# Performance work log

Measured on AMD Instinct MI355X. Metric: run time of the kernel, lower is better.

The kernel has to match this reference:

```python
import jax, jax.numpy as jnp
import numpy as np

EMBED_DIM = 1024
NUM_HEADS = 16
HEAD_DIM = EMBED_DIM // NUM_HEADS
ROPE_BASE = 10000.0


def _rope_cos_sin(seq_len, head_dim, dtype):
    # Standard RoPE (ESM-style rotate_half): freqs outer(t, inv_freq), emb = cat(freqs, freqs)
    inv_freq = 1.0 / (ROPE_BASE ** (jnp.arange(0, head_dim, 2, dtype=jnp.float32) / head_dim))
    t = jnp.arange(seq_len, dtype=jnp.float32)
    freqs = jnp.einsum('s,d->sd', t, inv_freq)          # [s, d/2]
    emb = jnp.concatenate([freqs, freqs], axis=-1)      # [s, d]
    return jnp.cos(emb).astype(dtype), jnp.sin(emb).astype(dtype)


def _rotate_half(x):
    x1, x2 = jnp.split(x, 2, axis=-1)
    return jnp.concatenate([-x2, x1], axis=-1)


def _apply_rope(x, cos, sin):
    # x: [b, h, s, d]; cos/sin: [s, d] broadcast over b, h
    return x * cos + _rotate_half(x) * sin


def setup_inputs() -> dict:
    key = jax.random.key(0)
    ks = jax.random.split(key, 5)
    b, s, e = 4, 2048, EMBED_DIM
    scale = 1.0 / np.sqrt(e)
    x = jax.random.normal(ks[0], (b, s, e), dtype=jnp.float32)
    Wqkv = jax.random.normal(ks[1], (e, 3 * e), dtype=jnp.float32) * scale
    bqkv = jnp.zeros((3 * e,), dtype=jnp.float32)
    Wo = jax.random.normal(ks[2], (e, e), dtype=jnp.float32) * scale
    bo = jnp.zeros((e,), dtype=jnp.float32)
    return {"x": x, "Wqkv": Wqkv, "bqkv": bqkv, "Wo": Wo, "bo": bo}


def reference(x, Wqkv, bqkv, Wo, bo):
    b, s, e = x.shape
    h, d = NUM_HEADS, HEAD_DIM
    qkv = jnp.einsum('bse,ef->bsf', x, Wqkv) + bqkv          # [b, s, 3e]
    q, k, v = jnp.split(qkv, 3, axis=-1)
    # b s (h d) -> b h s d
    q = q.reshape(b, s, h, d).transpose(0, 2, 1, 3)
    k = k.reshape(b, s, h, d).transpose(0, 2, 1, 3)
    v = v.reshape(b, s, h, d).transpose(0, 2, 1, 3)
    cos, sin = _rope_cos_sin(s, d, x.dtype)
    q = _apply_rope(q, cos, sin)
    k = _apply_rope(k, cos, sin)
    # scaled dot product attention (no mask, no dropout, non-causal)
    scores = jnp.einsum('bhqd,bhkd->bhqk', q, k) / jnp.asarray(np.sqrt(d), x.dtype)
    attn = jax.nn.softmax(scores, axis=-1)
    out = jnp.einsum('bhqk,bhkd->bhqd', attn, v)             # [b, h, s, d]
    out = out.transpose(0, 2, 1, 3).reshape(b, s, e)         # b h s d -> b s (h d)
    return jnp.einsum('bse,ef->bsf', out, Wo) + bo
```

## Files before the change

kernel.cpp:

```cpp
#include <hip/hip_runtime.h>
#include <stdint.h>
#include <stddef.h>

typedef __bf16 bf16;
typedef __attribute__((ext_vector_type(8))) __bf16 bf16x8;
typedef __attribute__((ext_vector_type(4))) __bf16 bf16x4;
typedef __attribute__((ext_vector_type(4))) float f32x4;
typedef __attribute__((ext_vector_type(4))) float float4v;

#define BATCH 4
#define SEQ   2048
#define EMB   1024
#define NH    16
#define HD    64
#define F3    3072

#define MFMA16(a, b, c) __builtin_amdgcn_mfma_f32_16x16x32_bf16((a), (b), (c), 0, 0, 0)

__device__ __forceinline__ void gload_lds16(const bf16* g, bf16* l) {
  __builtin_amdgcn_global_load_lds(
      (const __attribute__((address_space(1))) uint32_t*)g,
      (__attribute__((address_space(3))) uint32_t*)l, 16, 0, 0);
}

__global__ __launch_bounds__(256) void rope_table(float* __restrict__ cosT,
                                                  float* __restrict__ sinT) {
  int idx = blockIdx.x * 256 + threadIdx.x;
  int pos = idx >> 5, d1 = idx & 31;
  float inv = powf(10000.0f, -(float)(2 * d1) / 64.0f);
  float th = (float)pos * inv;
  cosT[idx] = cosf(th);
  sinT[idx] = sinf(th);
}

__global__ __launch_bounds__(256) void convert_bf16(const float* __restrict__ src,
                                                    bf16* __restrict__ dst, int n4) {
  int i = blockIdx.x * 256 + threadIdx.x;
  if (i >= n4) return;
  float4v v = ((const float4v*)src)[i];
  bf16x4 o;
#pragma unroll
  for (int k = 0; k < 4; ++k) o[k] = (bf16)v[k];
  ((bf16x4*)dst)[i] = o;
}

__global__ __launch_bounds__(256) void transpose_f32_bf16(const float* __restrict__ in,
                                                          bf16* __restrict__ out,
                                                          int R, int C) {
  __shared__ bf16 tile[32][33];
  const int tx = threadIdx.x & 31;
  const int ty = threadIdx.x >> 5;
  const int c0 = blockIdx.x * 32, r0 = blockIdx.y * 32;
#pragma unroll
  for (int kk = 0; kk < 4; ++kk) {
    int r = ty + kk * 8;
    tile[r][tx] = (bf16)in[(size_t)(r0 + r) * C + c0 + tx];
  }
  __syncthreads();
#pragma unroll
  for (int kk = 0; kk < 4; ++kk) {
    int r = ty + kk * 8;
    out[(size_t)(c0 + r) * R + r0 + tx] = tile[tx][r];
  }
}

__global__ __launch_bounds__(256) void qkv_rope_kernel(
    const bf16* __restrict__ x, const bf16* __restrict__ wT,
    const float* __restrict__ bias, bf16* __restrict__ qo, bf16* __restrict__ ko,
    bf16* __restrict__ vo, const float* __restrict__ cosT,
    const float* __restrict__ sinT) {
  __shared__ __align__(16) bf16 As[128 * 32];
  __shared__ __align__(16) bf16 Bs[128 * 32];
  const int tid = threadIdx.x;
  const int w = tid >> 6, lane = tid & 63;
  const int lhi = lane >> 4, llo = lane & 15;
  const int wr = w >> 1, wc = w & 1;
  const int row_a0 = blockIdx.y * 128;
  const int row_b0 = blockIdx.x * 128;

  f32x4 acc[4][4];
#pragma unroll
  for (int i = 0; i < 4; ++i)
#pragma unroll
    for (int j = 0; j < 4; ++j) acc[i][j] = (f32x4){0.f, 0.f, 0.f, 0.f};

  for (int k0 = 0; k0 < EMB; k0 += 32) {
#pragma unroll
    for (int c = 0; c < 2; ++c) {
      int chunk = w * 2 + c;
      int gl = chunk * 64 + lane;
      int row = gl >> 2, kk = (gl & 3) << 3;
      gload_lds16(x + (size_t)(row_a0 + row) * EMB + k0 + kk, &As[chunk * 512]);
      gload_lds16(wT + (size_t)(row_b0 + row) * EMB + k0 + kk, &Bs[chunk * 512]);
    }
    __syncthreads();
    bf16x8 a[4], b[4];
#pragma unroll
    for (int i = 0; i < 4; ++i)
      a[i] = *(const bf16x8*)&As[(wr * 64 + i * 16 + llo) * 32 + lhi * 8];
#pragma unroll
    for (int j = 0; j < 4; ++j)
      b[j] = *(const bf16x8*)&Bs[(wc * 64 + j * 16 + llo) * 32 + lhi * 8];
#pragma unroll
    for (int i = 0; i < 4; ++i)
#pragma unroll
      for (int j = 0; j < 4; ++j) acc[i][j] = MFMA16(a[i], b[j], acc[i][j]);
    __syncthreads();
  }

  const int f0 = row_b0 + wc * 64;
  const int part = f0 >> 10;
  const int hh = (f0 & 1023) >> 6;
  const int m_base = row_a0 + wr * 64;

  float bvals[4];
#pragma unroll
  for (int j = 0; j < 4; ++j) bvals[j] = bias[f0 + j * 16 + llo];

  if (part == 2) {
#pragma unroll
    for (int i = 0; i < 4; ++i) {
      int m0 = m_base + i * 16 + lhi * 4;
      int bb = m0 >> 11, pos0 = m0 & 2047;
#pragma unroll
      for (int j = 0; j < 4; ++j) {
        int dd = j * 16 + llo;
        bf16x4 pk;
#pragma unroll
        for (int r = 0; r < 4; ++r) pk[r] = (bf16)(acc[i][j][r] + bvals[j]);
        *(bf16x4*)(vo + ((size_t)(bb * NH + hh) * HD + dd) * SEQ + pos0) = pk;
      }
    }
  } else {
    bf16* dst = (part == 0) ? qo : ko;
    const float qs = (part == 0) ? 0.125f : 1.0f;
#pragma unroll
    for (int i = 0; i < 4; ++i) {
#pragma unroll
      for (int r = 0; r < 4; ++r) {
        int m = m_base + i * 16 + lhi * 4 + r;
        int bb = m >> 11, pos = m & 2047;
        size_t base = ((size_t)(bb * NH + hh) * SEQ + pos) * HD;
#pragma unroll
        for (int j = 0; j < 2; ++j) {
          int d1 = j * 16 + llo;
          float x1 = acc[i][j][r] + bvals[j];
          float x2 = acc[i][j + 2][r] + bvals[j + 2];
          float cth = cosT[pos * 32 + d1];
          float sth = sinT[pos * 32 + d1];
          dst[base + d1] = (bf16)((x1 * cth - x2 * sth) * qs);
          dst[base + d1 + 32] = (bf16)((x2 * cth + x1 * sth) * qs);
        }
      }
    }
  }
}

__global__ __launch_bounds__(512) void attn_kernel(const bf16* __restrict__ q,
                                                   const bf16* __restrict__ k,
                                                   const bf16* __restrict__ vT,
                                                   bf16* __restrict__ o) {
  __shared__ __align__(16) bf16 smem[32768];
  bf16* Qs = smem;

  const int tid = threadIdx.x, w = tid >> 6, lane = tid & 63;
  const int lhi = lane >> 4, llo = lane & 15;
  const int l7 = llo & 7;
  const int bidx = blockIdx.x;
  const int vblk = (bidx & 7) * 64 + (bidx >> 3);
  const int qt = vblk & 7, bh = vblk >> 3;
  const bf16* qbase = q + (size_t)bh * SEQ * HD + qt * 256 * HD;
  const bf16* kbase = k + (size_t)bh * SEQ * HD;
  const bf16* vbase = vT + (size_t)bh * HD * SEQ;
  bf16* Pw = smem + w * 2048;

  const int rowc = lane >> 3;
  const int sw8 = (lane & 7) ^ rowc;

#pragma unroll
  for (int c = 0; c < 4; ++c) {
    int chunk = w * 4 + c;
    int row = chunk * 8 + rowc;
    gload_lds16(qbase + (size_t)row * HD + sw8 * 8, &Qs[chunk * 512]);
  }
  if (w < 4) {
#pragma unroll
    for (int c = 0; c < 2; ++c) {
      int chunk = w * 2 + c;
      int row = chunk * 8 + rowc;
      gload_lds16(kbase + (size_t)row * HD + sw8 * 8, &smem[16384 + chunk * 512]);
    }
  } else {
#pragma unroll
    for (int c = 0; c < 2; ++c) {
      int chunk = (w - 4) * 2 + c;
      int row = chunk * 8 + rowc;
      gload_lds16(vbase + (size_t)row * SEQ + sw8 * 8, &smem[24576 + chunk * 512]);
    }
  }
  __syncthreads();

  bf16x8 qf[2][2];
#pragma unroll
  for (int i = 0; i < 2; ++i)
#pragma unroll
    for (int kc = 0; kc < 2; ++kc)
      qf[i][kc] = *(const bf16x8*)&Qs[(w * 32 + i * 16 + llo) * 64 +
                                      (((kc * 4 + lhi) ^ l7) * 8)];
  __syncthreads();

  float rsum[2] = {0.f, 0.f};
  f32x4 oacc[2][4];
#pragma unroll
  for (int i = 0; i < 2; ++i)
#pragma unroll
    for (int j = 0; j < 4; ++j) oacc[i][j] = (f32x4){0.f, 0.f, 0.f, 0.f};

  for (int kb = 0; kb < 32; ++kb) {
    bf16* Kc = smem + 16384 + (kb & 1) * 4096;
    bf16* Vc = smem + 24576 + (kb & 1) * 4096;
    if (kb < 31) {
      int kpos = (kb + 1) * 64;
      if (w < 4) {
        bf16* Kn = smem + 16384 + ((kb + 1) & 1) * 4096;
#pragma unroll
        for (int c = 0; c < 2; ++c) {
          int chunk = w * 2 + c;
          int row = chunk * 8 + rowc;
          gload_lds16(kbase + (size_t)(kpos + row) * HD + sw8 * 8, &Kn[chunk * 512]);
        }
      } else {
        bf16* Vn = smem + 24576 + ((kb + 1) & 1) * 4096;
#pragma unroll
        for (int c = 0; c < 2; ++c) {
          int chunk = (w - 4) * 2 + c;
          int row = chunk * 8 + rowc;
          gload_lds16(vbase + (size_t)row * SEQ + kpos + sw8 * 8, &Vn[chunk * 512]);
        }
      }
    }
    f32x4 st[4][2];
#pragma unroll
    for (int tt = 0; tt < 4; ++tt)
#pragma unroll
      for (int i = 0; i < 2; ++i) st[tt][i] = (f32x4){0.f, 0.f, 0.f, 0.f};
#pragma unroll
    for (int kc = 0; kc < 2; ++kc) {
      bf16x8 kfr[4];
#pragma unroll
      for (int tt = 0; tt < 4; ++tt)
        kfr[tt] = *(const bf16x8*)&Kc[(tt * 16 + llo) * 64 +
                                      (((kc * 4 + lhi) ^ l7) * 8)];
#pragma unroll
      for (int tt = 0; tt < 4; ++tt)
#pragma unroll
        for (int i = 0; i < 2; ++i)
          st[tt][i] = MFMA16(kfr[tt], qf[i][kc], st[tt][i]);
    }
#pragma unroll
    for (int tt = 0; tt < 4; ++tt) {
#pragma unroll
      for (int i = 0; i < 2; ++i) {
        bf16x4 pk;
        float a = 0.f;
#pragma unroll
        for (int r = 0; r < 4; ++r) {
          float p = __expf(st[tt][i][r]);
          pk[r] = (bf16)p;
          a += p;
        }
        rsum[i] += a;
        int gi = (tt * 4 + lhi) ^ (l7 << 1);
        *(bf16x4*)&Pw[(i * 16 + llo) * 64 + gi * 4] = pk;
      }
    }
#pragma unroll
    for (int kc = 0; kc < 2; ++kc) {
      bf16x8 af[2], bv[4];
      int xg = ((kc * 4 + lhi) ^ l7) * 8;
      int pg = ((kc * 8 + lhi * 2) ^ (l7 << 1)) * 4;
#pragma unroll
      for (int i = 0; i < 2; ++i)
        af[i] = *(const bf16x8*)&Pw[(i * 16 + llo) * 64 + pg];
#pragma unroll
      for (int jd = 0; jd < 4; ++jd)
        bv[jd] = *(const bf16x8*)&Vc[(jd * 16 + llo) * 64 + xg];
#pragma unroll
      for (int i = 0; i < 2; ++i)
#pragma unroll
        for (int jd = 0; jd < 4; ++jd) oacc[i][jd] = MFMA16(af[i], bv[jd], oacc[i][jd]);
    }
    __syncthreads();
  }

  const int bb = bh >> 4, hh = bh & 15;
#pragma unroll
  for (int i = 0; i < 2; ++i) {
    float t = rsum[i];
    t += __shfl_xor(t, 16);
    t += __shfl_xor(t, 32);
#pragma unroll
    for (int r = 0; r < 4; ++r) {
      float l = __shfl(t, lhi * 4 + r);
      float inv = 1.0f / l;
      int pos = qt * 256 + w * 32 + i * 16 + lhi * 4 + r;
      size_t base = ((size_t)bb * SEQ + pos) * EMB + hh * HD;
#pragma unroll
      for (int jd = 0; jd < 4; ++jd)
        o[base + jd * 16 + llo] = (bf16)(oacc[i][jd][r] * inv);
    }
  }
}

__global__ __launch_bounds__(256) void outproj_kernel(const bf16* __restrict__ a_in,
                                                      const bf16* __restrict__ wT,
                                                      const float* __restrict__ bo,
                                                      float* __restrict__ out) {
  __shared__ __align__(16) bf16 As[128 * 32];
  __shared__ __align__(16) bf16 Bs[128 * 32];
  const int tid = threadIdx.x;
  const int w = tid >> 6, lane = tid & 63;
  const int lhi = lane >> 4, llo = lane & 15;
  const int wr = w >> 1, wc = w & 1;
  const int row_a0 = blockIdx.y * 128;
  const int row_b0 = blockIdx.x * 128;

  f32x4 acc[4][4];
#pragma unroll
  for (int i = 0; i < 4; ++i)
#pragma unroll
    for (int j = 0; j < 4; ++j) acc[i][j] = (f32x4){0.f, 0.f, 0.f, 0.f};

  for (int k0 = 0; k0 < EMB; k0 += 32) {
#pragma unroll
    for (int c = 0; c < 2; ++c) {
      int chunk = w * 2 + c;
      int gl = chunk * 64 + lane;
      int row = gl >> 2, kk = (gl & 3) << 3;
      gload_lds16(a_in + (size_t)(row_a0 + row) * EMB + k0 + kk, &As[chunk * 512]);
      gload_lds16(wT + (size_t)(row_b0 + row) * EMB + k0 + kk, &Bs[chunk * 512]);
    }
    __syncthreads();
    bf16x8 a[4], b[4];
#pragma unroll
    for (int i = 0; i < 4; ++i)
      a[i] = *(const bf16x8*)&As[(wr * 64 + i * 16 + llo) * 32 + lhi * 8];
#pragma unroll
    for (int j = 0; j < 4; ++j)
      b[j] = *(const bf16x8*)&Bs[(wc * 64 + j * 16 + llo) * 32 + lhi * 8];
#pragma unroll
    for (int i = 0; i < 4; ++i)
#pragma unroll
      for (int j = 0; j < 4; ++j) acc[i][j] = MFMA16(a[i], b[j], acc[i][j]);
    __syncthreads();
  }

  const int col0 = row_b0 + wc * 64;
  const int m_base = row_a0 + wr * 64;
  float bvals[4];
#pragma unroll
  for (int j = 0; j < 4; ++j) bvals[j] = bo[col0 + j * 16 + llo];
#pragma unroll
  for (int i = 0; i < 4; ++i) {
#pragma unroll
    for (int r = 0; r < 4; ++r) {
      int m = m_base + i * 16 + lhi * 4 + r;
#pragma unroll
      for (int j = 0; j < 4; ++j)
        out[(size_t)m * EMB + col0 + j * 16 + llo] = acc[i][j][r] + bvals[j];
    }
  }
}

extern "C" void kernel_launch(void* const* d_in, const int* in_sizes, int n_in,
                              void* d_out, int out_size, void* d_ws, size_t ws_size,
                              hipStream_t stream) {
  const float* x_raw = (const float*)d_in[0];
  const float* wqkv_raw = (const float*)d_in[1];
  const float* bqkv = (const float*)d_in[2];
  const float* wo_raw = (const float*)d_in[3];
  const float* bo = (const float*)d_in[4];
  float* out = (float*)d_out;

  char* ws = (char*)d_ws;
  bf16* qw = (bf16*)(ws);
  bf16* kw = (bf16*)(ws + 16777216);
  bf16* vw = (bf16*)(ws + 33554432);
  bf16* wqkvT = (bf16*)(ws + 50331648);
  float* cosT = (float*)(ws + 56623104);
  float* sinT = (float*)(ws + 56885248);
  bf16* ow = (bf16*)(ws + 50331648);
  bf16* woT = (bf16*)(ws);
  bf16* xb = (bf16*)d_out;

  rope_table<<<256, 256, 0, stream>>>(cosT, sinT);
  convert_bf16<<<(BATCH * SEQ * EMB / 4 + 255) / 256, 256, 0, stream>>>(
      x_raw, xb, BATCH * SEQ * EMB / 4);
  transpose_f32_bf16<<<dim3(F3 / 32, EMB / 32), 256, 0, stream>>>(wqkv_raw, wqkvT, EMB, F3);

  qkv_rope_kernel<<<dim3(F3 / 128, (BATCH * SEQ) / 128), 256, 0, stream>>>(
      xb, wqkvT, bqkv, qw, kw, vw, cosT, sinT);
  attn_kernel<<<dim3(BATCH * NH * (SEQ / 256)), 512, 0, stream>>>(qw, kw, vw, ow);

  transpose_f32_bf16<<<dim3(EMB / 32, EMB / 32), 256, 0, stream>>>(wo_raw, woT, EMB, EMB);
  outproj_kernel<<<dim3(EMB / 128, (BATCH * SEQ) / 128), 256, 0, stream>>>(
      ow, woT, bo, out);
}
```

Before: 292.0 us.

## Halve attention block to 4 waves, each owning 64 query rows

```diff
diff --git a/kernel.cpp b/kernel.cpp
--- a/kernel.cpp
+++ b/kernel.cpp
@@ -156,7 +156,7 @@
   }
 }
 
-__global__ __launch_bounds__(512) void attn_kernel(const bf16* __restrict__ q,
+__global__ __launch_bounds__(256) void attn_kernel(const bf16* __restrict__ q,
                                                    const bf16* __restrict__ k,
                                                    const bf16* __restrict__ vT,
                                                    bf16* __restrict__ o) {
@@ -172,142 +172,128 @@
   const bf16* qbase = q + (size_t)bh * SEQ * HD + qt * 256 * HD;
   const bf16* kbase = k + (size_t)bh * SEQ * HD;
   const bf16* vbase = vT + (size_t)bh * HD * SEQ;
-  bf16* Pw = smem + w * 2048;
+  bf16* Pw = smem + w * 4096;
 
   const int rowc = lane >> 3;
   const int sw8 = (lane & 7) ^ rowc;
 
 #pragma unroll
-  for (int c = 0; c < 4; ++c) {
-    int chunk = w * 4 + c;
+  for (int c = 0; c < 8; ++c) {
+    int chunk = w * 8 + c;
     int row = chunk * 8 + rowc;
     gload_lds16(qbase + (size_t)row * HD + sw8 * 8, &Qs[chunk * 512]);
   }
-  if (w < 4) {
-#pragma unroll
-    for (int c = 0; c < 2; ++c) {
-      int chunk = w * 2 + c;
-      int row = chunk * 8 + rowc;
-      gload_lds16(kbase + (size_t)row * HD + sw8 * 8, &smem[16384 + chunk * 512]);
-    }
-  } else {
-#pragma unroll
-    for (int c = 0; c < 2; ++c) {
-      int chunk = (w - 4) * 2 + c;
-      int row = chunk * 8 + rowc;
-      gload_lds16(vbase + (size_t)row * SEQ + sw8 * 8, &smem[24576 + chunk * 512]);
-    }
+#pragma unroll
+  for (int c = 0; c < 2; ++c) {
+    int chunk = w * 2 + c;
+    int row = chunk * 8 + rowc;
+    gload_lds16(kbase + (size_t)row * HD + sw8 * 8, &smem[16384 + chunk * 512]);
+    gload_lds16(vbase + (size_t)row * SEQ + sw8 * 8, &smem[24576 + chunk * 512]);
   }
   __syncthreads();
 
-  bf16x8 qf[2][2];
-#pragma unroll
-  for (int i = 0; i < 2; ++i)
+  bf16x8 qf[4][2];
+#pragma unroll
+  for (int qi = 0; qi < 4; ++qi)
 #pragma unroll
     for (int kc = 0; kc < 2; ++kc)
-      qf[i][kc] = *(const bf16x8*)&Qs[(w * 32 + i * 16 + llo) * 64 +
-                                      (((kc * 4 + lhi) ^ l7) * 8)];
-  __syncthreads();
-
-  float rsum[2] = {0.f, 0.f};
-  f32x4 oacc[2][4];
-#pragma unroll
-  for (int i = 0; i < 2; ++i)
-#pragma unroll
-    for (int j = 0; j < 4; ++j) oacc[i][j] = (f32x4){0.f, 0.f, 0.f, 0.f};
+      qf[qi][kc] = *(const bf16x8*)&Qs[(w * 64 + qi * 16 + llo) * 64 +
+                                       (((kc * 4 + lhi) ^ l7) * 8)];
+
+  float rsum[4] = {0.f, 0.f, 0.f, 0.f};
+  f32x4 oacc[4][4];
+#pragma unroll
+  for (int qi = 0; qi < 4; ++qi)
+#pragma unroll
+    for (int jd = 0; jd < 4; ++jd) oacc[qi][jd] = (f32x4){0.f, 0.f, 0.f, 0.f};
 
   for (int kb = 0; kb < 32; ++kb) {
     bf16* Kc = smem + 16384 + (kb & 1) * 4096;
     bf16* Vc = smem + 24576 + (kb & 1) * 4096;
     if (kb < 31) {
+      bf16* Kn = smem + 16384 + ((kb + 1) & 1) * 4096;
+      bf16* Vn = smem + 24576 + ((kb + 1) & 1) * 4096;
       int kpos = (kb + 1) * 64;
-      if (w < 4) {
-        bf16* Kn = smem + 16384 + ((kb + 1) & 1) * 4096;
-#pragma unroll
-        for (int c = 0; c < 2; ++c) {
-          int chunk = w * 2 + c;
-          int row = chunk * 8 + rowc;
-          gload_lds16(kbase + (size_t)(kpos + row) * HD + sw8 * 8, &Kn[chunk * 512]);
+#pragma unroll
+      for (int c = 0; c < 2; ++c) {
+        int chunk = w * 2 + c;
+        int row = chunk * 8 + rowc;
+        gload_lds16(kbase + (size_t)(kpos + row) * HD + sw8 * 8, &Kn[chunk * 512]);
+        gload_lds16(vbase + (size_t)row * SEQ + kpos + sw8 * 8, &Vn[chunk * 512]);
+      }
+    }
+#pragma unroll
+    for (int th = 0; th < 2; ++th) {
+      f32x4 st[2][4];
+#pragma unroll
+      for (int t2 = 0; t2 < 2; ++t2)
+#pragma unroll
+        for (int qi = 0; qi < 4; ++qi) st[t2][qi] = (f32x4){0.f, 0.f, 0.f, 0.f};
+#pragma unroll
+      for (int kc = 0; kc < 2; ++kc) {
+        bf16x8 kfr[2];
+#pragma unroll
+        for (int t2 = 0; t2 < 2; ++t2)
+          kfr[t2] = *(const bf16x8*)&Kc[((th * 2 + t2) * 16 + llo) * 64 +
+                                        (((kc * 4 + lhi) ^ l7) * 8)];
+#pragma unroll
+        for (int t2 = 0; t2 < 2; ++t2)
+#pragma unroll
+          for (int qi = 0; qi < 4; ++qi)
+            st[t2][qi] = MFMA16(kfr[t2], qf[qi][kc], st[t2][qi]);
+      }
+#pragma unroll
+      for (int t2 = 0; t2 < 2; ++t2) {
+#pragma unroll
+        for (int qi = 0; qi < 4; ++qi) {
+          bf16x4 pk;
+          float a = 0.f;
+#pragma unroll
+          for (int r = 0; r < 4; ++r) {
+            float p = __expf(st[t2][qi][r]);
+            pk[r] = (bf16)p;
+            a += p;
+          }
+          rsum[qi] += a;
+          int sg = (th * 8 + t2 * 4 + lhi) ^ (l7 << 1);
+          *(bf16x4*)&Pw[(qi * 16 + llo) * 64 + sg * 4] = pk;
         }
-      } else {
-        bf16* Vn = smem + 24576 + ((kb + 1) & 1) * 4096;
-#pragma unroll
-        for (int c = 0; c < 2; ++c) {
-          int chunk = (w - 4) * 2 + c;
-          int row = chunk * 8 + rowc;
-          gload_lds16(vbase + (size_t)row * SEQ + kpos + sw8 * 8, &Vn[chunk * 512]);
-        }
-      }
-    }
-    f32x4 st[4][2];
-#pragma unroll
-    for (int tt = 0; tt < 4; ++tt)
-#pragma unroll
-      for (int i = 0; i < 2; ++i) st[tt][i] = (f32x4){0.f, 0.f, 0.f, 0.f};
+      }
+    }
 #pragma unroll
     for (int kc = 0; kc < 2; ++kc) {
-      bf16x8 kfr[4];
-#pragma unroll
-      for (int tt = 0; tt < 4; ++tt)
-        kfr[tt] = *(const bf16x8*)&Kc[(tt * 16 + llo) * 64 +
-                                      (((kc * 4 + lhi) ^ l7) * 8)];
-#pragma unroll
-      for (int tt = 0; tt < 4; ++tt)
-#pragma unroll
-        for (int i = 0; i < 2; ++i)
-          st[tt][i] = MFMA16(kfr[tt], qf[i][kc], st[tt][i]);
-    }
-#pragma unroll
-    for (int tt = 0; tt < 4; ++tt) {
-#pragma unroll
-      for (int i = 0; i < 2; ++i) {
-        bf16x4 pk;
-        float a = 0.f;
-#pragma unroll
-        for (int r = 0; r < 4; ++r) {
-          float p = __expf(st[tt][i][r]);
-          pk[r] = (bf16)p;
-          a += p;
-        }
-        rsum[i] += a;
-        int gi = (tt * 4 + lhi) ^ (l7 << 1);
-        *(bf16x4*)&Pw[(i * 16 + llo) * 64 + gi * 4] = pk;
-      }
-    }
-#pragma unroll
-    for (int kc = 0; kc < 2; ++kc) {
-      bf16x8 af[2], bv[4];
+      bf16x8 af[4], bv[4];
       int xg = ((kc * 4 + lhi) ^ l7) * 8;
-      int pg = ((kc * 8 + lhi * 2) ^ (l7 << 1)) * 4;
-#pragma unroll
-      for (int i = 0; i < 2; ++i)
-        af[i] = *(const bf16x8*)&Pw[(i * 16 + llo) * 64 + pg];
+#pragma unroll
+      for (int qi = 0; qi < 4; ++qi)
+        af[qi] = *(const bf16x8*)&Pw[(qi * 16 + llo) * 64 + xg];
 #pragma unroll
       for (int jd = 0; jd < 4; ++jd)
         bv[jd] = *(const bf16x8*)&Vc[(jd * 16 + llo) * 64 + xg];
 #pragma unroll
-      for (int i = 0; i < 2; ++i)
-#pragma unroll
-        for (int jd = 0; jd < 4; ++jd) oacc[i][jd] = MFMA16(af[i], bv[jd], oacc[i][jd]);
+      for (int qi = 0; qi < 4; ++qi)
+#pragma unroll
+        for (int jd = 0; jd < 4; ++jd)
+          oacc[qi][jd] = MFMA16(af[qi], bv[jd], oacc[qi][jd]);
     }
     __syncthreads();
   }
 
   const int bb = bh >> 4, hh = bh & 15;
 #pragma unroll
-  for (int i = 0; i < 2; ++i) {
-    float t = rsum[i];
+  for (int qi = 0; qi < 4; ++qi) {
+    float t = rsum[qi];
     t += __shfl_xor(t, 16);
     t += __shfl_xor(t, 32);
 #pragma unroll
     for (int r = 0; r < 4; ++r) {
       float l = __shfl(t, lhi * 4 + r);
       float inv = 1.0f / l;
-      int pos = qt * 256 + w * 32 + i * 16 + lhi * 4 + r;
+      int pos = qt * 256 + w * 64 + qi * 16 + lhi * 4 + r;
       size_t base = ((size_t)bb * SEQ + pos) * EMB + hh * HD;
 #pragma unroll
       for (int jd = 0; jd < 4; ++jd)
-        o[base + jd * 16 + llo] = (bf16)(oacc[i][jd][r] * inv);
+        o[base + jd * 16 + llo] = (bf16)(oacc[qi][jd][r] * inv);
     }
   }
 }
@@ -400,7 +386,7 @@
 
   qkv_rope_kernel<<<dim3(F3 / 128, (BATCH * SEQ) / 128), 256, 0, stream>>>(
       xb, wqkvT, bqkv, qw, kw, vw, cosT, sinT);
-  attn_kernel<<<dim3(BATCH * NH * (SEQ / 256)), 512, 0, stream>>>(qw, kw, vw, ow);
+  attn_kernel<<<dim3(BATCH * NH * (SEQ / 256)), 256, 0, stream>>>(qw, kw, vw, ow);
 
   transpose_f32_bf16<<<dim3(EMB / 32, EMB / 32), 256, 0, stream>>>(wo_raw, woT, EMB, EMB);
   outproj_kernel<<<dim3(EMB / 128, (BATCH * SEQ) / 128), 256, 0, stream>>>(
```

New measurement: 297.3 us. About the same (+1.8%).
